# Kernel tuning notes

Hardware: AMD Instinct MI355X
Metric: run time of the kernel (lower is better)

The kernel has to match this reference:

```python
import jax, jax.numpy as jnp
import numpy as np


def setup_inputs() -> dict:
    key = jax.random.key(0)
    k1, k2, k3 = jax.random.split(key, 3)
    B, Sq, Sk, H, Hk, D = 2, 2048, 2048, 16, 4, 64
    q = jax.random.normal(k1, (B, Sq, H, D), dtype=jnp.float32)
    kv = jax.random.normal(k2, (B, Sk, 2, Hk, D), dtype=jnp.float32)
    key_padding_mask = jax.random.randint(k3, (B, Sk), 0, 2).astype(bool)
    return {"q": q, "kv": kv, "key_padding_mask": key_padding_mask}


def reference(q, kv, key_padding_mask):
    # q: (B, Sq, H, D); kv: (B, Sk, 2, Hk, D); key_padding_mask: (B, Sk) bool (True = keep)
    B, Sq, H, D = q.shape
    Hk = kv.shape[3]
    if Hk != H:
        # GQA: repeat kv heads so (... hkv d) -> (... (hkv g) d)
        kv = jnp.repeat(kv, H // Hk, axis=3)
    k = kv[:, :, 0]  # (B, Sk, H, D)
    v = kv[:, :, 1]  # (B, Sk, H, D)
    softmax_scale = 1.0 / jnp.sqrt(jnp.asarray(D, dtype=q.dtype))
    scores = jnp.einsum('bthd,bshd->bhts', q, k * softmax_scale)  # (B, H, Sq, Sk)
    # additive padding mask: 0 where keep, -10000 where masked (matches torch code)
    pad = jnp.where(key_padding_mask, jnp.asarray(0.0, scores.dtype),
                    jnp.asarray(-10000.0, scores.dtype))
    scores = scores + pad[:, None, None, :]
    attention = jax.nn.softmax(scores, axis=-1)
    # dropout rate is 0.0 -> identity
    output = jnp.einsum('bhts,bshd->bthd', attention, v)  # (B, Sq, H, D)
    return output
```

## Files before the change

kernel.cpp:

```cpp
#include <hip/hip_runtime.h>
#include <hip/hip_bf16.h>
#include <stdint.h>

typedef __bf16 bf16_t;
typedef bf16_t bf16x8 __attribute__((ext_vector_type(8)));
typedef bf16_t bf16x4 __attribute__((ext_vector_type(4)));
typedef float f32x4 __attribute__((ext_vector_type(4)));
typedef float f32x16 __attribute__((ext_vector_type(16)));
typedef uint32_t u32x4 __attribute__((ext_vector_type(4)));
typedef int   i32x4 __attribute__((ext_vector_type(4)));

#define BB 2
#define SQ 2048
#define SK 2048
#define NH 16
#define HKV 4
#define DD 64
#define GQ 4
#define MTILE 128
#define NTILE 64
#define MAXNT 32

#define KTILE_BYTES 8192
#define CNT_OFF   ((size_t)0)
#define KC_OFF    ((size_t)4096)
#define VC_OFF    (KC_OFF + (size_t)BB * HKV * MAXNT * KTILE_BYTES)

__device__ __forceinline__ int swz8(int row, int colByte) {
    return row * 128 + (colByte ^ ((row & 15) << 3));
}

#define GLDS(g, l) __builtin_amdgcn_global_load_lds( \
    (const __attribute__((address_space(1))) void*)(g), \
    (__attribute__((address_space(3))) void*)(l), 16, 0, 0)

__global__ __launch_bounds__(256)
void gather_kernel(const float* __restrict__ kv, const int* __restrict__ mask,
                   char* __restrict__ ws)
{
    __shared__ int wtot[4];
    __shared__ int cwin[NTILE];

    const int bid  = blockIdx.x;
    const int tile = bid & 31;
    const int bh   = bid >> 5;
    const int hk   = bh & 3;
    const int b    = bh >> 2;
    const int tid  = threadIdx.x;
    const int lane = tid & 63;
    const int wid  = tid >> 6;

    int m[8], c = 0;
    {
        const int base = b * SK + tid * 8;
        i32x4 a0 = *(const i32x4*)&mask[base];
        i32x4 a1 = *(const i32x4*)&mask[base + 4];
        #pragma unroll
        for (int j = 0; j < 4; ++j) { m[j] = a0[j] ? 1 : 0; c += m[j]; }
        #pragma unroll
        for (int j = 0; j < 4; ++j) { m[4 + j] = a1[j] ? 1 : 0; c += m[4 + j]; }
    }
    int sc = c;
    #pragma unroll
    for (int off = 1; off < 64; off <<= 1) {
        int n = __shfl_up(sc, off, 64);
        if (lane >= off) sc += n;
    }
    if (lane == 63) wtot[wid] = sc;
    __syncthreads();
    int wbase = 0;
    #pragma unroll
    for (int w = 0; w < 4; ++w) if (w < wid) wbase += wtot[w];
    const int cnt = wtot[0] + wtot[1] + wtot[2] + wtot[3];

    if (hk == 0 && tile == 0 && tid == 0)
        ((int*)(ws + CNT_OFF))[b] = cnt;

    const int w0 = tile * NTILE;
    int pos = wbase + sc - c;
    #pragma unroll
    for (int j = 0; j < 8; ++j)
        if (m[j]) {
            if (pos >= w0 && pos < w0 + NTILE) cwin[pos - w0] = tid * 8 + j;
            ++pos;
        }
    __syncthreads();

    const int nt = (cnt + 63) >> 6;
    if (tile >= nt) return;

    const int s4 = tid >> 4;
    const int d0 = (tid & 15) * 4;

    bf16_t* Kt = (bf16_t*)(ws + KC_OFF + (size_t)bid * KTILE_BYTES);
    bf16_t* Vt = (bf16_t*)(ws + VC_OFF + (size_t)bid * KTILE_BYTES);

    f32x4 kk4[4], vv4[4];
    #pragma unroll
    for (int p = 0; p < 4; ++p) {
        const int crow = w0 + s4 * 4 + p;
        if (crow < cnt) {
            const int s = cwin[s4 * 4 + p];
            const float* base = kv + (size_t)((b * SK + s) * 2) * (HKV * DD) + hk * DD + d0;
            kk4[p] = *(const f32x4*)base;
            vv4[p] = *(const f32x4*)(base + HKV * DD);
        } else {
            kk4[p] = (f32x4)(0.f);
            vv4[p] = (f32x4)(0.f);
        }
    }
    #pragma unroll
    for (int p = 0; p < 4; ++p) {
        bf16x4 kb;
        #pragma unroll
        for (int j = 0; j < 4; ++j) kb[j] = (bf16_t)kk4[p][j];
        *(bf16x4*)((char*)Kt + swz8(s4 * 4 + p, d0 * 2)) = kb;
    }
    #pragma unroll
    for (int j = 0; j < 4; ++j) {
        bf16x4 tv;
        #pragma unroll
        for (int p = 0; p < 4; ++p) tv[p] = (bf16_t)vv4[p][j];
        *(bf16x4*)((char*)Vt + swz8(d0 + j, s4 * 8)) = tv;
    }
}

__global__ __launch_bounds__(256, 2)
void fattn32p(const float* __restrict__ q, const char* __restrict__ ws,
              float* __restrict__ out)
{
    __shared__ __align__(16) bf16_t Ks[4][NTILE * 64];
    __shared__ __align__(16) bf16_t Vs[4][DD * 64];

    const int tid  = threadIdx.x;
    const int wid  = tid >> 6;
    const int lane = tid & 63;
    const int l31  = lane & 31;
    const int hf   = lane >> 5;

    const int bid = (blockIdx.x & 7) * 64 + (blockIdx.x >> 3);
    const int qt  = bid & 15;
    const int bh  = bid >> 4;
    const int hq  = bh & 15;
    const int b   = bh >> 4;
    const int hk  = hq / GQ;

    const int cnt = ((const int*)(ws + CNT_OFF))[b];
    const int nt  = (cnt + 63) >> 6;

    const int qrow0 = qt * MTILE + wid * 32;
    const float SC = 0.18033688011112042f;

    bf16x8 qf[4];
    {
        const float* qp = q + ((size_t)(b * SQ + qrow0 + l31) * NH + hq) * DD;
        #pragma unroll
        for (int kblk = 0; kblk < 4; ++kblk) {
            f32x4 v0 = *(const f32x4*)(qp + kblk * 16 + hf * 8);
            f32x4 v1 = *(const f32x4*)(qp + kblk * 16 + hf * 8 + 4);
            #pragma unroll
            for (int j = 0; j < 4; ++j) {
                qf[kblk][j]     = (bf16_t)(v0[j] * SC);
                qf[kblk][4 + j] = (bf16_t)(v1[j] * SC);
            }
        }
    }

    const char* kgb = ws + KC_OFF + (size_t)((b * HKV + hk) * MAXNT) * KTILE_BYTES;
    const char* vgb = ws + VC_OFF + (size_t)((b * HKV + hk) * MAXNT) * KTILE_BYTES;

    auto STAGE = [&](int t, int buf) {
        const char* ksrc = kgb + (size_t)t * KTILE_BYTES + wid * 2048 + lane * 16;
        const char* vsrc = vgb + (size_t)t * KTILE_BYTES + wid * 2048 + lane * 16;
        char* kdst = (char*)Ks[buf] + wid * 2048;
        char* vdst = (char*)Vs[buf] + wid * 2048;
        GLDS(ksrc, kdst);
        GLDS(ksrc + 1024, kdst + 1024);
        GLDS(vsrc, vdst);
        GLDS(vsrc + 1024, vdst + 1024);
    };

    auto LD8 = [&](const bf16_t* T, int row, int cB) -> bf16x8 {
        const char* p = (const char*)T + row * 128;
        const int x = (row & 15) << 3;
        union { bf16x4 h[2]; bf16x8 v; } u;
        u.h[0] = *(const bf16x4*)(p + (cB ^ x));
        u.h[1] = *(const bf16x4*)(p + ((cB + 8) ^ x));
        return u.v;
    };

    f32x16 o0, o1;
    #pragma unroll
    for (int i = 0; i < 16; ++i) { o0[i] = 0.f; o1[i] = 0.f; }
    float l_run = 0.f;

    auto QK = [&](int t, int buf, f32x16& s0, f32x16& s1) {
        if (t == nt - 1) {
            #pragma unroll
            for (int i = 0; i < 16; ++i) {
                const int sl = (i & 3) + 8 * (i >> 2) + 4 * hf;
                s0[i] = (t * 64 + sl      < cnt) ? 0.f : -30000.f;
                s1[i] = (t * 64 + sl + 32 < cnt) ? 0.f : -30000.f;
            }
        } else {
            #pragma unroll
            for (int i = 0; i < 16; ++i) { s0[i] = 0.f; s1[i] = 0.f; }
        }
        __builtin_amdgcn_s_setprio(1);
        #pragma unroll
        for (int kblk = 0; kblk < 4; ++kblk) {
            bf16x8 kf0 = LD8(Ks[buf], l31,      kblk * 32 + hf * 16);
            bf16x8 kf1 = LD8(Ks[buf], 32 + l31, kblk * 32 + hf * 16);
            s0 = __builtin_amdgcn_mfma_f32_32x32x16_bf16(kf0, qf[kblk], s0, 0, 0, 0);
            s1 = __builtin_amdgcn_mfma_f32_32x32x16_bf16(kf1, qf[kblk], s1, 0, 0, 0);
        }
        __builtin_amdgcn_s_setprio(0);
    };

    auto SM = [&](f32x16& s0, f32x16& s1, bf16x8* paw) {
        #pragma unroll
        for (int i = 0; i < 16; ++i) {
            s0[i] = __builtin_amdgcn_exp2f(s0[i]);
            s1[i] = __builtin_amdgcn_exp2f(s1[i]);
        }
        float t0 = 0.f, t1 = 0.f, t2 = 0.f, t3 = 0.f;
        #pragma unroll
        for (int i = 0; i < 4; ++i) {
            t0 += s0[i]      + s1[i];
            t1 += s0[4 + i]  + s1[4 + i];
            t2 += s0[8 + i]  + s1[8 + i];
            t3 += s0[12 + i] + s1[12 + i];
        }
        l_run += (t0 + t1) + (t2 + t3);

        #pragma unroll
        for (int ks2 = 0; ks2 < 4; ++ks2) {
            const int aX = (ks2 & 1) * 2;
            uint32_t X0, X1, Y0, Y1;
            #define CVTPK(dst, lo, hi) asm("v_cvt_pk_bf16_f32 %0, %1, %2" : "=v"(dst) : "v"(lo), "v"(hi))
            if (ks2 & 2) {
                CVTPK(X0, s1[4*aX + 0], s1[4*aX + 1]);
                CVTPK(X1, s1[4*aX + 2], s1[4*aX + 3]);
                CVTPK(Y0, s1[4*aX + 4], s1[4*aX + 5]);
                CVTPK(Y1, s1[4*aX + 6], s1[4*aX + 7]);
            } else {
                CVTPK(X0, s0[4*aX + 0], s0[4*aX + 1]);
                CVTPK(X1, s0[4*aX + 2], s0[4*aX + 3]);
                CVTPK(Y0, s0[4*aX + 4], s0[4*aX + 5]);
                CVTPK(Y1, s0[4*aX + 6], s0[4*aX + 7]);
            }
            #undef CVTPK
            asm("v_permlane32_swap_b32 %0, %1" : "+v"(X0), "+v"(Y0));
            asm("v_permlane32_swap_b32 %0, %1" : "+v"(X1), "+v"(Y1));
            union { u32x4 w; bf16x8 v; } u;
            u.w[0] = X0; u.w[1] = X1; u.w[2] = Y0; u.w[3] = Y1;
            paw[ks2] = u.v;
        }
    };

    auto PV = [&](int buf, const bf16x8* paw) {
        __builtin_amdgcn_s_setprio(1);
        #pragma unroll
        for (int ks2 = 0; ks2 < 4; ++ks2) {
            bf16x8 vf0 = LD8(Vs[buf], l31,      ks2 * 32 + hf * 16);
            bf16x8 vf1 = LD8(Vs[buf], 32 + l31, ks2 * 32 + hf * 16);
            o0 = __builtin_amdgcn_mfma_f32_32x32x16_bf16(paw[ks2], vf0, o0, 0, 0, 0);
            o1 = __builtin_amdgcn_mfma_f32_32x32x16_bf16(paw[ks2], vf1, o1, 0, 0, 0);
        }
        __builtin_amdgcn_s_setprio(0);
    };

    STAGE(0, 0);
    if (1 < nt) STAGE(1, 1);

    int t = 0;
    for (; t + 1 < nt; t += 2) {
        const int n2 = (t + 2 < nt) ? 1 : 0;
        const int n3 = (t + 3 < nt) ? 1 : 0;
        if (n2) STAGE(t + 2, (t + 2) & 3);
        if (n3) STAGE(t + 3, (t + 3) & 3);
        if (n2 + n3 == 2)      asm volatile("s_waitcnt vmcnt(8)" ::: "memory");
        else if (n2 + n3 == 1) asm volatile("s_waitcnt vmcnt(4)" ::: "memory");
        else                   asm volatile("s_waitcnt vmcnt(0)" ::: "memory");
        __builtin_amdgcn_s_barrier();
        __builtin_amdgcn_sched_barrier(0);

        f32x16 sA0, sA1, sB0, sB1;
        bf16x8 pawA[4], pawB[4];
        QK(t,     t & 3,       sA0, sA1);
        QK(t + 1, (t + 1) & 3, sB0, sB1);
        SM(sA0, sA1, pawA);
        PV(t & 3, pawA);
        SM(sB0, sB1, pawB);
        PV((t + 1) & 3, pawB);

        __builtin_amdgcn_sched_barrier(0);
        __builtin_amdgcn_s_barrier();
    }
    if (t < nt) {
        asm volatile("s_waitcnt vmcnt(0)" ::: "memory");
        __builtin_amdgcn_s_barrier();
        __builtin_amdgcn_sched_barrier(0);
        f32x16 sA0, sA1;
        bf16x8 pawA[4];
        QK(t, t & 3, sA0, sA1);
        SM(sA0, sA1, pawA);
        PV(t & 3, pawA);
    }

    float lt = l_run + __shfl_xor(l_run, 32, 64);
    #pragma unroll
    for (int r = 0; r < 16; ++r) {
        const int t_r = (r & 3) + 8 * (r >> 2) + 4 * hf;
        const float den = __shfl(lt, t_r, 64);
        const float linv = den > 0.f ? 1.f / den : 0.f;
        float* op = out + ((size_t)(b * SQ + qrow0 + t_r) * NH + hq) * DD + l31;
        op[0]  = o0[r] * linv;
        op[32] = o1[r] * linv;
    }
}

extern "C" void kernel_launch(void* const* d_in, const int* in_sizes, int n_in,
                              void* d_out, int out_size, void* d_ws, size_t ws_size,
                              hipStream_t stream) {
    const float* q    = (const float*)d_in[0];
    const float* kv   = (const float*)d_in[1];
    const int*   mask = (const int*)d_in[2];
    float* out = (float*)d_out;

    gather_kernel<<<BB * HKV * MAXNT, 256, 0, stream>>>(kv, mask, (char*)d_ws);
    fattn32p<<<BB * NH * (SQ / MTILE), 256, 0, stream>>>(q, (const char*)d_ws, out);
}
```

Baseline: 39.85 us.

## Switch attention kernel to 16x16 MFMA with smaller query tiles and LDS P

Replaces the 32x32x16 MFMA attention kernel with a 16x16x32 variant that gives each wave 16 query rows, halving the query tile to 64 and doubling the grid. The softmax probabilities now pass through a per-wave LDS buffer instead of register permlane swaps. The K/V pipeline drops from a four-buffer, two-tiles-per-iteration scheme to a simple double buffer, and occupancy is raised to 4 blocks per CU. The aim is more parallelism and lower register pressure, at the cost of twice as many K/V tile loads in total and extra LDS round trips for P.

```diff
diff --git a/kernel.cpp b/kernel.cpp
--- a/kernel.cpp
+++ b/kernel.cpp
@@ -6,7 +6,6 @@
 typedef bf16_t bf16x8 __attribute__((ext_vector_type(8)));
 typedef bf16_t bf16x4 __attribute__((ext_vector_type(4)));
 typedef float f32x4 __attribute__((ext_vector_type(4)));
-typedef float f32x16 __attribute__((ext_vector_type(16)));
 typedef uint32_t u32x4 __attribute__((ext_vector_type(4)));
 typedef int   i32x4 __attribute__((ext_vector_type(4)));
 
@@ -17,7 +16,7 @@
 #define HKV 4
 #define DD 64
 #define GQ 4
-#define MTILE 128
+#define MTILE 64
 #define NTILE 64
 #define MAXNT 32
 
@@ -125,22 +124,23 @@
     }
 }
 
-__global__ __launch_bounds__(256, 2)
-void fattn32p(const float* __restrict__ q, const char* __restrict__ ws,
-              float* __restrict__ out)
+__global__ __launch_bounds__(256, 4)
+void fattn16(const float* __restrict__ q, const char* __restrict__ ws,
+             float* __restrict__ out)
 {
-    __shared__ __align__(16) bf16_t Ks[4][NTILE * 64];
-    __shared__ __align__(16) bf16_t Vs[4][DD * 64];
+    __shared__ __align__(16) bf16_t Ks[2][NTILE * 64];
+    __shared__ __align__(16) bf16_t Vs[2][DD * 64];
+    __shared__ __align__(16) bf16_t Ps[4][16 * 64];
 
     const int tid  = threadIdx.x;
     const int wid  = tid >> 6;
     const int lane = tid & 63;
-    const int l31  = lane & 31;
-    const int hf   = lane >> 5;
-
-    const int bid = (blockIdx.x & 7) * 64 + (blockIdx.x >> 3);
-    const int qt  = bid & 15;
-    const int bh  = bid >> 4;
+    const int l16  = lane & 15;
+    const int lg   = lane >> 4;
+
+    const int bid = (blockIdx.x & 7) * 128 + (blockIdx.x >> 3);
+    const int qt  = bid & 31;
+    const int bh  = bid >> 5;
     const int hq  = bh & 15;
     const int b   = bh >> 4;
     const int hk  = hq / GQ;
@@ -148,20 +148,20 @@
     const int cnt = ((const int*)(ws + CNT_OFF))[b];
     const int nt  = (cnt + 63) >> 6;
 
-    const int qrow0 = qt * MTILE + wid * 32;
+    const int qrow0 = qt * MTILE + wid * 16;
     const float SC = 0.18033688011112042f;
 
-    bf16x8 qf[4];
+    bf16x8 qf[2];
     {
-        const float* qp = q + ((size_t)(b * SQ + qrow0 + l31) * NH + hq) * DD;
-        #pragma unroll
-        for (int kblk = 0; kblk < 4; ++kblk) {
-            f32x4 v0 = *(const f32x4*)(qp + kblk * 16 + hf * 8);
-            f32x4 v1 = *(const f32x4*)(qp + kblk * 16 + hf * 8 + 4);
+        const float* qp = q + ((size_t)(b * SQ + qrow0 + l16) * NH + hq) * DD;
+        #pragma unroll
+        for (int kk = 0; kk < 2; ++kk) {
+            f32x4 v0 = *(const f32x4*)(qp + kk * 32 + lg * 8);
+            f32x4 v1 = *(const f32x4*)(qp + kk * 32 + lg * 8 + 4);
             #pragma unroll
             for (int j = 0; j < 4; ++j) {
-                qf[kblk][j]     = (bf16_t)(v0[j] * SC);
-                qf[kblk][4 + j] = (bf16_t)(v1[j] * SC);
+                qf[kk][j]     = (bf16_t)(v0[j] * SC);
+                qf[kk][4 + j] = (bf16_t)(v1[j] * SC);
             }
         }
     }
@@ -189,134 +189,90 @@
         return u.v;
     };
 
-    f32x16 o0, o1;
-    #pragma unroll
-    for (int i = 0; i < 16; ++i) { o0[i] = 0.f; o1[i] = 0.f; }
+    f32x4 o_acc[4];
+    #pragma unroll
+    for (int i = 0; i < 4; ++i) o_acc[i] = (f32x4)(0.f);
     float l_run = 0.f;
 
-    auto QK = [&](int t, int buf, f32x16& s0, f32x16& s1) {
-        if (t == nt - 1) {
-            #pragma unroll
-            for (int i = 0; i < 16; ++i) {
-                const int sl = (i & 3) + 8 * (i >> 2) + 4 * hf;
-                s0[i] = (t * 64 + sl      < cnt) ? 0.f : -30000.f;
-                s1[i] = (t * 64 + sl + 32 < cnt) ? 0.f : -30000.f;
-            }
-        } else {
-            #pragma unroll
-            for (int i = 0; i < 16; ++i) { s0[i] = 0.f; s1[i] = 0.f; }
-        }
-        __builtin_amdgcn_s_setprio(1);
-        #pragma unroll
-        for (int kblk = 0; kblk < 4; ++kblk) {
-            bf16x8 kf0 = LD8(Ks[buf], l31,      kblk * 32 + hf * 16);
-            bf16x8 kf1 = LD8(Ks[buf], 32 + l31, kblk * 32 + hf * 16);
-            s0 = __builtin_amdgcn_mfma_f32_32x32x16_bf16(kf0, qf[kblk], s0, 0, 0, 0);
-            s1 = __builtin_amdgcn_mfma_f32_32x32x16_bf16(kf1, qf[kblk], s1, 0, 0, 0);
-        }
-        __builtin_amdgcn_s_setprio(0);
-    };
-
-    auto SM = [&](f32x16& s0, f32x16& s1, bf16x8* paw) {
-        #pragma unroll
-        for (int i = 0; i < 16; ++i) {
-            s0[i] = __builtin_amdgcn_exp2f(s0[i]);
-            s1[i] = __builtin_amdgcn_exp2f(s1[i]);
-        }
-        float t0 = 0.f, t1 = 0.f, t2 = 0.f, t3 = 0.f;
-        #pragma unroll
-        for (int i = 0; i < 4; ++i) {
-            t0 += s0[i]      + s1[i];
-            t1 += s0[4 + i]  + s1[4 + i];
-            t2 += s0[8 + i]  + s1[8 + i];
-            t3 += s0[12 + i] + s1[12 + i];
-        }
-        l_run += (t0 + t1) + (t2 + t3);
-
-        #pragma unroll
-        for (int ks2 = 0; ks2 < 4; ++ks2) {
-            const int aX = (ks2 & 1) * 2;
-            uint32_t X0, X1, Y0, Y1;
-            #define CVTPK(dst, lo, hi) asm("v_cvt_pk_bf16_f32 %0, %1, %2" : "=v"(dst) : "v"(lo), "v"(hi))
-            if (ks2 & 2) {
-                CVTPK(X0, s1[4*aX + 0], s1[4*aX + 1]);
-                CVTPK(X1, s1[4*aX + 2], s1[4*aX + 3]);
-                CVTPK(Y0, s1[4*aX + 4], s1[4*aX + 5]);
-                CVTPK(Y1, s1[4*aX + 6], s1[4*aX + 7]);
-            } else {
-                CVTPK(X0, s0[4*aX + 0], s0[4*aX + 1]);
-                CVTPK(X1, s0[4*aX + 2], s0[4*aX + 3]);
-                CVTPK(Y0, s0[4*aX + 4], s0[4*aX + 5]);
-                CVTPK(Y1, s0[4*aX + 6], s0[4*aX + 7]);
-            }
-            #undef CVTPK
-            asm("v_permlane32_swap_b32 %0, %1" : "+v"(X0), "+v"(Y0));
-            asm("v_permlane32_swap_b32 %0, %1" : "+v"(X1), "+v"(Y1));
-            union { u32x4 w; bf16x8 v; } u;
-            u.w[0] = X0; u.w[1] = X1; u.w[2] = Y0; u.w[3] = Y1;
-            paw[ks2] = u.v;
-        }
-    };
-
-    auto PV = [&](int buf, const bf16x8* paw) {
-        __builtin_amdgcn_s_setprio(1);
-        #pragma unroll
-        for (int ks2 = 0; ks2 < 4; ++ks2) {
-            bf16x8 vf0 = LD8(Vs[buf], l31,      ks2 * 32 + hf * 16);
-            bf16x8 vf1 = LD8(Vs[buf], 32 + l31, ks2 * 32 + hf * 16);
-            o0 = __builtin_amdgcn_mfma_f32_32x32x16_bf16(paw[ks2], vf0, o0, 0, 0, 0);
-            o1 = __builtin_amdgcn_mfma_f32_32x32x16_bf16(paw[ks2], vf1, o1, 0, 0, 0);
-        }
-        __builtin_amdgcn_s_setprio(0);
-    };
-
     STAGE(0, 0);
-    if (1 < nt) STAGE(1, 1);
-
-    int t = 0;
-    for (; t + 1 < nt; t += 2) {
-        const int n2 = (t + 2 < nt) ? 1 : 0;
-        const int n3 = (t + 3 < nt) ? 1 : 0;
-        if (n2) STAGE(t + 2, (t + 2) & 3);
-        if (n3) STAGE(t + 3, (t + 3) & 3);
-        if (n2 + n3 == 2)      asm volatile("s_waitcnt vmcnt(8)" ::: "memory");
-        else if (n2 + n3 == 1) asm volatile("s_waitcnt vmcnt(4)" ::: "memory");
-        else                   asm volatile("s_waitcnt vmcnt(0)" ::: "memory");
-        __builtin_amdgcn_s_barrier();
-        __builtin_amdgcn_sched_barrier(0);
-
-        f32x16 sA0, sA1, sB0, sB1;
-        bf16x8 pawA[4], pawB[4];
-        QK(t,     t & 3,       sA0, sA1);
-        QK(t + 1, (t + 1) & 3, sB0, sB1);
-        SM(sA0, sA1, pawA);
-        PV(t & 3, pawA);
-        SM(sB0, sB1, pawB);
-        PV((t + 1) & 3, pawB);
-
-        __builtin_amdgcn_sched_barrier(0);
-        __builtin_amdgcn_s_barrier();
-    }
-    if (t < nt) {
+
+    for (int t = 0; t < nt; ++t) {
+        const int cur = t & 1;
         asm volatile("s_waitcnt vmcnt(0)" ::: "memory");
         __builtin_amdgcn_s_barrier();
         __builtin_amdgcn_sched_barrier(0);
-        f32x16 sA0, sA1;
-        bf16x8 pawA[4];
-        QK(t, t & 3, sA0, sA1);
-        SM(sA0, sA1, pawA);
-        PV(t & 3, pawA);
-    }
-
-    float lt = l_run + __shfl_xor(l_run, 32, 64);
-    #pragma unroll
-    for (int r = 0; r < 16; ++r) {
-        const int t_r = (r & 3) + 8 * (r >> 2) + 4 * hf;
+        if (t + 1 < nt) STAGE(t + 1, cur ^ 1);
+
+        f32x4 sacc[4];
+        if (t == nt - 1) {
+            #pragma unroll
+            for (int nb = 0; nb < 4; ++nb)
+                #pragma unroll
+                for (int r = 0; r < 4; ++r)
+                    sacc[nb][r] = (t * 64 + nb * 16 + lg * 4 + r < cnt) ? 0.f : -30000.f;
+        } else {
+            #pragma unroll
+            for (int nb = 0; nb < 4; ++nb) sacc[nb] = (f32x4)(0.f);
+        }
+        __builtin_amdgcn_s_setprio(1);
+        #pragma unroll
+        for (int nb = 0; nb < 4; ++nb) {
+            #pragma unroll
+            for (int kk = 0; kk < 2; ++kk) {
+                bf16x8 kf = LD8(Ks[cur], nb * 16 + l16, kk * 64 + lg * 16);
+                sacc[nb] = __builtin_amdgcn_mfma_f32_16x16x32_bf16(kf, qf[kk], sacc[nb], 0, 0, 0);
+            }
+        }
+        __builtin_amdgcn_s_setprio(0);
+
+        #pragma unroll
+        for (int nb = 0; nb < 4; ++nb) {
+            #pragma unroll
+            for (int r = 0; r < 4; ++r)
+                sacc[nb][r] = __builtin_amdgcn_exp2f(sacc[nb][r]);
+        }
+        {
+            float t0 = 0.f, t1 = 0.f;
+            #pragma unroll
+            for (int r = 0; r < 4; ++r) {
+                t0 += sacc[0][r] + sacc[1][r];
+                t1 += sacc[2][r] + sacc[3][r];
+            }
+            l_run += t0 + t1;
+        }
+        #pragma unroll
+        for (int nb = 0; nb < 4; ++nb) {
+            bf16x4 pb;
+            #pragma unroll
+            for (int r = 0; r < 4; ++r) pb[r] = (bf16_t)sacc[nb][r];
+            *(bf16x4*)((char*)Ps[wid] + swz8(l16, (nb * 16 + lg * 4) * 2)) = pb;
+        }
+        asm volatile("s_waitcnt lgkmcnt(0)" ::: "memory");
+
+        __builtin_amdgcn_s_setprio(1);
+        #pragma unroll
+        for (int ks = 0; ks < 2; ++ks) {
+            bf16x8 pa = LD8(Ps[wid], l16, ks * 64 + lg * 16);
+            #pragma unroll
+            for (int dc = 0; dc < 4; ++dc) {
+                bf16x8 vb = LD8(Vs[cur], dc * 16 + l16, ks * 64 + lg * 16);
+                o_acc[dc] = __builtin_amdgcn_mfma_f32_16x16x32_bf16(pa, vb, o_acc[dc], 0, 0, 0);
+            }
+        }
+        __builtin_amdgcn_s_setprio(0);
+    }
+
+    float lt = l_run + __shfl_xor(l_run, 16, 64);
+    lt += __shfl_xor(lt, 32, 64);
+    #pragma unroll
+    for (int r = 0; r < 4; ++r) {
+        const int t_r = lg * 4 + r;
         const float den = __shfl(lt, t_r, 64);
         const float linv = den > 0.f ? 1.f / den : 0.f;
-        float* op = out + ((size_t)(b * SQ + qrow0 + t_r) * NH + hq) * DD + l31;
-        op[0]  = o0[r] * linv;
-        op[32] = o1[r] * linv;
+        float* op = out + ((size_t)(b * SQ + qrow0 + t_r) * NH + hq) * DD;
+        #pragma unroll
+        for (int dc = 0; dc < 4; ++dc)
+            op[dc * 16 + l16] = o_acc[dc][r] * linv;
     }
 }
 
@@ -329,5 +285,5 @@
     float* out = (float*)d_out;
 
     gather_kernel<<<BB * HKV * MAXNT, 256, 0, stream>>>(kv, mask, (char*)d_ws);
-    fattn32p<<<BB * NH * (SQ / MTILE), 256, 0, stream>>>(q, (const char*)d_ws, out);
-}
+    fattn16<<<BB * NH * (SQ / MTILE), 256, 0, stream>>>(q, (const char*)d_ws, out);
+}
```

New measurement: 45.27 us. +13.6%, slower.
